# Kernel optimization log

Measured on AMD Instinct MI355X. Metric: run time of the kernel, lower is better.

Reference implementation:

```python
import jax, jax.numpy as jnp
import numpy as np

N = 50000        # nodes
E = 800000       # edges
H = 128          # hidden_channels
NH = 4           # num_heads
HD = H // NH     # head_dim
EPS = 1e-5       # LayerNorm eps (torch default)


def setup_inputs() -> dict:
    key = jax.random.key(0)
    ks = jax.random.split(key, 16)
    s = 0.02
    return {
        "x": jax.random.normal(ks[0], (N, H), dtype=jnp.float32),
        "edge_index": jax.random.randint(ks[1], (2, E), 0, N, dtype=jnp.int64),
        "Wq": jax.random.normal(ks[2], (H, H), dtype=jnp.float32) * s,
        "bq": jnp.zeros((H,), jnp.float32),
        "Wk": jax.random.normal(ks[3], (H, H), dtype=jnp.float32) * s,
        "bk": jnp.zeros((H,), jnp.float32),
        "Wv": jax.random.normal(ks[4], (H, H), dtype=jnp.float32) * s,
        "bv": jnp.zeros((H,), jnp.float32),
        "W1": jax.random.normal(ks[5], (2 * H, H), dtype=jnp.float32) * s,
        "b1": jnp.zeros((H,), jnp.float32),
        "ln_g": jnp.ones((H,), jnp.float32),
        "ln_b": jnp.zeros((H,), jnp.float32),
        "W2": jax.random.normal(ks[6], (H, H), dtype=jnp.float32) * s,
        "b2": jnp.zeros((H,), jnp.float32),
    }


def reference(x, edge_index, Wq, bq, Wk, bk, Wv, bv, W1, b1, ln_g, ln_b, W2, b2):
    n = x.shape[0]
    row, col = edge_index[0], edge_index[1]
    # dense projections, split heads: [N, NH, HD]
    Q = (x @ Wq + bq).reshape(n, NH, HD)
    K = (x @ Wk + bk).reshape(n, NH, HD)
    V = (x @ Wv + bv).reshape(n, NH, HD)
    # edge-wise gather + per-head dot product: [E, NH]
    scores = (Q[row] * K[col]).sum(-1) / jnp.sqrt(jnp.float32(HD))
    # segment softmax over edges grouped by destination node (row)
    m = jax.ops.segment_max(scores, row, num_segments=n)        # [N, NH]
    m = jnp.where(jnp.isfinite(m), m, 0.0)                      # empty segments -> 0
    e = jnp.exp(scores - m[row])                                # [E, NH]
    denom = jax.ops.segment_sum(e, row, num_segments=n)         # [N, NH]
    w = e / denom[row]                                          # [E, NH]
    # weighted scatter-add aggregation: [N, H]
    msg = (w[..., None] * V[col]).reshape(-1, NH * HD)          # [E, H]
    agg = jax.ops.segment_sum(msg, row, num_segments=n)         # [N, H]
    # MLP: Linear -> ReLU -> LayerNorm -> Linear, plus residual
    h = jax.nn.relu(jnp.concatenate([x, agg], axis=-1) @ W1 + b1)
    mu = h.mean(-1, keepdims=True)
    var = ((h - mu) ** 2).mean(-1, keepdims=True)
    h = (h - mu) / jnp.sqrt(var + EPS) * ln_g + ln_b
    return h @ W2 + b2 + x
```

## Files before the change

### kernel.cpp

```cpp
#include <hip/hip_runtime.h>
#include <hip/hip_bf16.h>

#define NN 50000
#define HH 128
#define NHEAD 4
#define HD 32
#define EE 800000
#define LN_EPS 1e-5f
#define ROWS_PAD 50048
#define SCAN_NB 98

typedef __bf16 bf16x8 __attribute__((ext_vector_type(8)));
typedef short  s16x8  __attribute__((ext_vector_type(8)));
typedef float  f32x4  __attribute__((ext_vector_type(4)));

__device__ __forceinline__ f32x4 mfma_bf16(s16x8 a, s16x8 b, f32x4 c) {
    return __builtin_amdgcn_mfma_f32_16x16x32_bf16((bf16x8)a, (bf16x8)b, c, 0, 0, 0);
}

__device__ __forceinline__ unsigned short f2bf(float f) {
    union { float f; unsigned int u; } v; v.f = f;
    unsigned int u = v.u + 0x7FFFu + ((v.u >> 16) & 1u);
    return (unsigned short)(u >> 16);
}

__global__ void detect_idx_kernel(const unsigned int* __restrict__ buf, int* __restrict__ flag) {
    if (blockIdx.x == 0 && threadIdx.x == 0) {
        int is64 = 1;
        for (int i = 0; i < 64; ++i) {
            if (buf[2 * i + 1] != 0u) { is64 = 0; break; }
        }
        *flag = is64;
    }
}

__global__ void convert_hist_kernel(const void* __restrict__ ei, const int* __restrict__ flag,
                                    int* __restrict__ rowi, int* __restrict__ coli,
                                    int* __restrict__ deg) {
    int i = blockIdx.x * blockDim.x + threadIdx.x;
    if (i >= EE) return;
    int r, c;
    if (*flag) {
        const long long* p = (const long long*)ei;
        r = (int)p[i];
        c = (int)p[EE + i];
    } else {
        const int* p = (const int*)ei;
        r = p[i];
        c = p[EE + i];
    }
    rowi[i] = r;
    coli[i] = c;
    atomicAdd(&deg[r], 1);
}

__global__ __launch_bounds__(512) void scan_a_kernel(const int* __restrict__ deg,
                                                     int* __restrict__ bsum) {
    __shared__ int red[8];
    const int t = threadIdx.x;
    const int gid = blockIdx.x * 512 + t;
    int v = (gid < NN) ? deg[gid] : 0;
    #pragma unroll
    for (int o = 1; o < 64; o <<= 1) v += __shfl_xor(v, o);
    if ((t & 63) == 0) red[t >> 6] = v;
    __syncthreads();
    if (t == 0) {
        int s = 0;
        #pragma unroll
        for (int k = 0; k < 8; ++k) s += red[k];
        bsum[blockIdx.x] = s;
    }
}

__global__ void scan_b_kernel(const int* __restrict__ bsum, int* __restrict__ boff) {
    const int lane = threadIdx.x;
    const int i0 = lane * 2, i1 = lane * 2 + 1;
    int a = (i0 < SCAN_NB) ? bsum[i0] : 0;
    int b = (i1 < SCAN_NB) ? bsum[i1] : 0;
    int incl = a + b;
    const int own = incl;
    #pragma unroll
    for (int o = 1; o < 64; o <<= 1) {
        int u = __shfl_up(incl, o);
        if (lane >= o) incl += u;
    }
    int excl = incl - own;
    if (i0 < SCAN_NB) boff[i0] = excl;
    if (i1 < SCAN_NB) boff[i1] = excl + a;
}

__global__ __launch_bounds__(512) void scan_c_kernel(const int* __restrict__ deg,
                                                     const int* __restrict__ boff,
                                                     int* __restrict__ rstart,
                                                     int* __restrict__ cursor) {
    __shared__ int wsum[8];
    const int t = threadIdx.x;
    const int gid = blockIdx.x * 512 + t;
    const int lane = t & 63, w = t >> 6;
    int v = (gid < NN) ? deg[gid] : 0;
    int incl = v;
    #pragma unroll
    for (int o = 1; o < 64; o <<= 1) {
        int u = __shfl_up(incl, o);
        if (lane >= o) incl += u;
    }
    if (lane == 63) wsum[w] = incl;
    __syncthreads();
    int woff = 0;
    for (int k = 0; k < w; ++k) woff += wsum[k];
    int excl = boff[blockIdx.x] + woff + incl - v;
    if (gid < NN) { rstart[gid] = excl; cursor[gid] = excl; }
    if (gid == 0) rstart[NN] = EE;
}

__global__ void scatter_kernel(const int* __restrict__ rowi, const int* __restrict__ coli,
                               int* __restrict__ cursor, int* __restrict__ colS) {
    int i = blockIdx.x * blockDim.x + threadIdx.x;
    if (i >= EE) return;
    int pos = atomicAdd(&cursor[rowi[i]], 1);
    colS[pos] = coli[i];
}

#define PACKX_T 1600000
__global__ void pack_kernel(const float* __restrict__ x,
                            const float* __restrict__ Wq, const float* __restrict__ Wk,
                            const float* __restrict__ Wv, const float* __restrict__ W1,
                            const float* __restrict__ W2,
                            unsigned short* __restrict__ xa, unsigned short* __restrict__ wf) {
    int t = blockIdx.x * blockDim.x + threadIdx.x;
    if (t < PACKX_T) {
        int r = t >> 5;
        int c4 = (t & 31) << 2;
        float4 v = *(const float4*)(x + (size_t)r * HH + c4);
        ushort4 o;
        o.x = f2bf(v.x); o.y = f2bf(v.y); o.z = f2bf(v.z); o.w = f2bf(v.w);
        *(ushort4*)(xa + (size_t)r * 256 + c4) = o;
        return;
    }
    int i = t - PACKX_T;
    if (i >= 98304) return;
    float val;
    if (i < 49152) {
        int j = i & 7, lane = (i >> 3) & 63, kk = (i >> 9) & 3, nt = i >> 11;
        int k = kk * 32 + (lane >> 4) * 8 + j;
        int n = nt * 16 + (lane & 15);
        const float* W = (n < 128) ? Wq : ((n < 256) ? Wk : Wv);
        val = W[k * HH + (n & 127)];
    } else if (i < 81920) {
        int local = i - 49152;
        int j = local & 7, lane = (local >> 3) & 63, kk = (local >> 9) & 7, nt = local >> 12;
        int k = kk * 32 + (lane >> 4) * 8 + j;
        int n = nt * 16 + (lane & 15);
        val = W1[k * HH + n];
    } else {
        int local = i - 81920;
        int j = local & 7, lane = (local >> 3) & 63, kk = (local >> 9) & 3, nt = local >> 11;
        int k = kk * 32 + (lane >> 4) * 8 + j;
        int n = nt * 16 + (lane & 15);
        val = W2[k * HH + n];
    }
    wf[i] = f2bf(val);
}

__global__ __launch_bounds__(256) void gemm_qkv_kernel(
        const unsigned short* __restrict__ xa, const unsigned short* __restrict__ wf,
        const float* __restrict__ bq, const float* __restrict__ bk, const float* __restrict__ bv,
        unsigned short* __restrict__ Qb, unsigned short* __restrict__ Kb,
        unsigned short* __restrict__ Vb) {
    const int wave = threadIdx.x >> 6, lane = threadIdx.x & 63;
    const int row0 = blockIdx.x * 64 + wave * 16;
    const int arow = row0 + (lane & 15);

    s16x8 a[4];
    const unsigned short* ap = xa + (size_t)arow * 256 + (lane >> 4) * 8;
    #pragma unroll
    for (int kk = 0; kk < 4; ++kk) a[kk] = *(const s16x8*)(ap + kk * 32);

    f32x4 acc[24];
    #pragma unroll
    for (int nt = 0; nt < 24; ++nt) acc[nt] = (f32x4){0.f, 0.f, 0.f, 0.f};

    const s16x8* wfv = (const s16x8*)wf;
    #pragma unroll
    for (int nt = 0; nt < 24; ++nt) {
        #pragma unroll
        for (int kk = 0; kk < 4; ++kk) {
            s16x8 b = wfv[(nt * 4 + kk) * 64 + lane];
            acc[nt] = mfma_bf16(a[kk], b, acc[nt]);
        }
    }

    const int colb = lane & 15;
    const int rbase = row0 + (lane >> 4) * 4;
    #pragma unroll
    for (int nt = 0; nt < 24; ++nt) {
        const int mtx = nt >> 3;
        const int nc = (nt & 7) * 16 + colb;
        const float* bias_p = (mtx == 0) ? bq : ((mtx == 1) ? bk : bv);
        unsigned short* O = (mtx == 0) ? Qb : ((mtx == 1) ? Kb : Vb);
        float bias = bias_p[nc];
        #pragma unroll
        for (int r = 0; r < 4; ++r)
            O[(size_t)(rbase + r) * 128 + nc] = f2bf(acc[nt][r] + bias);
    }
}

__global__ __launch_bounds__(256) void attn_kernel(
        const unsigned short* __restrict__ Qb, const unsigned short* __restrict__ Kb,
        const unsigned short* __restrict__ Vb, const int* __restrict__ rstart,
        const int* __restrict__ colS, unsigned short* __restrict__ xa) {
    const int wave = threadIdx.x >> 6;
    const int lane = threadIdx.x & 63;
    const int i = blockIdx.x * 4 + wave;
    if (i >= NN) return;
    const int h = lane & 3;
    const int le = lane >> 2;
    const int g = lane >> 4;
    const int e0 = rstart[i], e1 = rstart[i + 1];
    const int deg = e1 - e0;

    float qf[32];
    {
        const uint4* qp = (const uint4*)(Qb + (size_t)i * 128 + h * 32);
        #pragma unroll
        for (int cch = 0; cch < 4; ++cch) {
            uint4 qv = qp[cch];
            unsigned int w_[4] = {qv.x, qv.y, qv.z, qv.w};
            #pragma unroll
            for (int dd = 0; dd < 4; ++dd) {
                qf[cch * 8 + dd * 2]     = __uint_as_float(w_[dd] << 16);
                qf[cch * 8 + dd * 2 + 1] = __uint_as_float(w_[dd] & 0xffff0000u);
            }
        }
    }

    float m = -INFINITY, l = 0.f;
    float accx = 0.f, accy = 0.f;

    for (int c0 = 0; c0 < deg; c0 += 16) {
        const int cnt = min(16, deg - c0);
        int col = 0;
        float s = -INFINITY;
        if (le < cnt) {
            col = colS[e0 + c0 + le];
            const uint4* kp = (const uint4*)(Kb + (size_t)col * 128 + h * 32);
            float dot = 0.f;
            #pragma unroll
            for (int cch = 0; cch < 4; ++cch) {
                uint4 kv = kp[cch];
                unsigned int w_[4] = {kv.x, kv.y, kv.z, kv.w};
                #pragma unroll
                for (int dd = 0; dd < 4; ++dd) {
                    dot += qf[cch * 8 + dd * 2]     * __uint_as_float(w_[dd] << 16);
                    dot += qf[cch * 8 + dd * 2 + 1] * __uint_as_float(w_[dd] & 0xffff0000u);
                }
            }
            s = dot * 0.17677669529663689f;
        }
        float sm = s;
        sm = fmaxf(sm, __shfl_xor(sm, 4));
        sm = fmaxf(sm, __shfl_xor(sm, 8));
        sm = fmaxf(sm, __shfl_xor(sm, 16));
        sm = fmaxf(sm, __shfl_xor(sm, 32));
        const float mn = fmaxf(m, sm);
        const float p = (le < cnt) ? __expf(s - mn) : 0.f;
        float ps = p;
        ps += __shfl_xor(ps, 4);
        ps += __shfl_xor(ps, 8);
        ps += __shfl_xor(ps, 16);
        ps += __shfl_xor(ps, 32);
        const float fac = __expf(m - mn);
        l = l * fac + ps;
        m = mn;
        const float facbc = __shfl(fac, g);
        accx *= facbc;
        accy *= facbc;
        #pragma unroll
        for (int e = 0; e < 16; ++e) {
            const int   cbc = __shfl(col, 4 * e);
            const float pbc = __shfl(p, 4 * e + g);
            const unsigned int v2 =
                *(const unsigned int*)(Vb + (size_t)cbc * 128 + 2 * lane);
            accx += pbc * __uint_as_float(v2 << 16);
            accy += pbc * __uint_as_float(v2 & 0xffff0000u);
        }
    }

    const float lf = __shfl(l, g);
    const float rinv = (lf > 0.f) ? 1.f / lf : 0.f;
    const unsigned int outw =
        ((unsigned int)f2bf(accy * rinv) << 16) | (unsigned int)f2bf(accx * rinv);
    *(unsigned int*)(xa + (size_t)i * 256 + 128 + 2 * lane) = outw;
}

__global__ __launch_bounds__(256) void gemm_mlp1_kernel(
        const unsigned short* __restrict__ xa, const unsigned short* __restrict__ w1f,
        const float* __restrict__ b1, const float* __restrict__ ln_g,
        const float* __restrict__ ln_b, unsigned short* __restrict__ hb) {
    const int wave = threadIdx.x >> 6, lane = threadIdx.x & 63;
    const int row0 = blockIdx.x * 64 + wave * 16;
    const int arow = row0 + (lane & 15);

    s16x8 a[8];
    const unsigned short* ap = xa + (size_t)arow * 256 + (lane >> 4) * 8;
    #pragma unroll
    for (int kk = 0; kk < 8; ++kk) a[kk] = *(const s16x8*)(ap + kk * 32);

    f32x4 acc[8];
    #pragma unroll
    for (int nt = 0; nt < 8; ++nt) acc[nt] = (f32x4){0.f, 0.f, 0.f, 0.f};

    const s16x8* wfv = (const s16x8*)w1f;
    #pragma unroll
    for (int nt = 0; nt < 8; ++nt) {
        #pragma unroll
        for (int kk = 0; kk < 8; ++kk) {
            s16x8 b = wfv[(nt * 8 + kk) * 64 + lane];
            acc[nt] = mfma_bf16(a[kk], b, acc[nt]);
        }
    }

    const int colb = lane & 15;
    #pragma unroll
    for (int nt = 0; nt < 8; ++nt) {
        float bias = b1[nt * 16 + colb];
        #pragma unroll
        for (int r = 0; r < 4; ++r) {
            float v = acc[nt][r] + bias;
            acc[nt][r] = v > 0.f ? v : 0.f;
        }
    }
    float mu[4], rs[4];
    #pragma unroll
    for (int r = 0; r < 4; ++r) {
        float s = 0.f, q = 0.f;
        #pragma unroll
        for (int nt = 0; nt < 8; ++nt) { float v = acc[nt][r]; s += v; q += v * v; }
        #pragma unroll
        for (int msk = 1; msk < 16; msk <<= 1) {
            s += __shfl_xor(s, msk, 16);
            q += __shfl_xor(q, msk, 16);
        }
        float m_ = s * (1.f / 128.f);
        float var = q * (1.f / 128.f) - m_ * m_;
        mu[r] = m_;
        rs[r] = rsqrtf(var + LN_EPS);
    }
    const int rbase = row0 + (lane >> 4) * 4;
    #pragma unroll
    for (int nt = 0; nt < 8; ++nt) {
        int col = nt * 16 + colb;
        float g = ln_g[col], bb = ln_b[col];
        #pragma unroll
        for (int r = 0; r < 4; ++r) {
            float h = (acc[nt][r] - mu[r]) * rs[r] * g + bb;
            hb[(size_t)(rbase + r) * 128 + col] = f2bf(h);
        }
    }
}

__global__ __launch_bounds__(256) void gemm_mlp2_kernel(
        const unsigned short* __restrict__ hb, const unsigned short* __restrict__ w2f,
        const float* __restrict__ b2, const float* __restrict__ x,
        float* __restrict__ out) {
    const int wave = threadIdx.x >> 6, lane = threadIdx.x & 63;
    const int row0 = blockIdx.x * 64 + wave * 16;
    const int arow = row0 + (lane & 15);

    s16x8 a[4];
    const unsigned short* ap = hb + (size_t)arow * 128 + (lane >> 4) * 8;
    #pragma unroll
    for (int kk = 0; kk < 4; ++kk) a[kk] = *(const s16x8*)(ap + kk * 32);

    f32x4 acc[8];
    #pragma unroll
    for (int nt = 0; nt < 8; ++nt) acc[nt] = (f32x4){0.f, 0.f, 0.f, 0.f};

    const s16x8* wfv = (const s16x8*)w2f;
    #pragma unroll
    for (int nt = 0; nt < 8; ++nt) {
        #pragma unroll
        for (int kk = 0; kk < 4; ++kk) {
            s16x8 b = wfv[(nt * 4 + kk) * 64 + lane];
            acc[nt] = mfma_bf16(a[kk], b, acc[nt]);
        }
    }

    const int colb = lane & 15;
    const int rbase = row0 + (lane >> 4) * 4;
    #pragma unroll
    for (int nt = 0; nt < 8; ++nt) {
        int col = nt * 16 + colb;
        float bias = b2[col];
        #pragma unroll
        for (int r = 0; r < 4; ++r) {
            int row = rbase + r;
            if (row < NN)
                out[(size_t)row * 128 + col] = acc[nt][r] + bias + x[(size_t)row * 128 + col];
        }
    }
}

extern "C" void kernel_launch(void* const* d_in, const int* in_sizes, int n_in,
                              void* d_out, int out_size, void* d_ws, size_t ws_size,
                              hipStream_t stream) {
    const float* x    = (const float*)d_in[0];
    const void*  ei   = d_in[1];
    const float* Wq   = (const float*)d_in[2];
    const float* bq   = (const float*)d_in[3];
    const float* Wk   = (const float*)d_in[4];
    const float* bk   = (const float*)d_in[5];
    const float* Wv   = (const float*)d_in[6];
    const float* bv   = (const float*)d_in[7];
    const float* W1   = (const float*)d_in[8];
    const float* b1   = (const float*)d_in[9];
    const float* ln_g = (const float*)d_in[10];
    const float* ln_b = (const float*)d_in[11];
    const float* W2   = (const float*)d_in[12];
    const float* b2   = (const float*)d_in[13];
    float* out = (float*)d_out;

    char* ws = (char*)d_ws;
    size_t off = 0;
    auto alloc = [&](size_t bytes) {
        size_t o = off;
        off = (off + bytes + 255) & ~(size_t)255;
        return o;
    };
    size_t flag_o = alloc(sizeof(int));
    size_t rowi_o = alloc((size_t)EE * sizeof(int));
    size_t coli_o = alloc((size_t)EE * sizeof(int));
    size_t deg_o  = alloc((size_t)NN * sizeof(int));
    size_t cur_o  = alloc((size_t)NN * sizeof(int));
    size_t rs_o   = alloc((size_t)(NN + 1) * sizeof(int));
    size_t bsum_o = alloc((size_t)SCAN_NB * sizeof(int));
    size_t boff_o = alloc((size_t)SCAN_NB * sizeof(int));
    size_t colS_o = alloc((size_t)EE * sizeof(int));
    size_t xa_o   = alloc((size_t)ROWS_PAD * 256 * sizeof(unsigned short));
    size_t wf_o   = alloc((size_t)98304 * sizeof(unsigned short));
    size_t Qb_o   = alloc((size_t)ROWS_PAD * 128 * sizeof(unsigned short));
    size_t Kb_o   = alloc((size_t)ROWS_PAD * 128 * sizeof(unsigned short));
    size_t Vb_o   = alloc((size_t)ROWS_PAD * 128 * sizeof(unsigned short));
    size_t hb_o   = Qb_o;

    int* flag   = (int*)(ws + flag_o);
    int* rowi   = (int*)(ws + rowi_o);
    int* coli   = (int*)(ws + coli_o);
    int* deg    = (int*)(ws + deg_o);
    int* cursor = (int*)(ws + cur_o);
    int* rstart = (int*)(ws + rs_o);
    int* bsum   = (int*)(ws + bsum_o);
    int* boff   = (int*)(ws + boff_o);
    int* colS   = (int*)(ws + colS_o);
    unsigned short* xa = (unsigned short*)(ws + xa_o);
    unsigned short* wf = (unsigned short*)(ws + wf_o);
    unsigned short* Qb = (unsigned short*)(ws + Qb_o);
    unsigned short* Kb = (unsigned short*)(ws + Kb_o);
    unsigned short* Vb = (unsigned short*)(ws + Vb_o);
    unsigned short* hb = (unsigned short*)(ws + hb_o);

    hipMemsetAsync(ws + deg_o, 0, (size_t)NN * sizeof(int), stream);

    detect_idx_kernel<<<1, 64, 0, stream>>>((const unsigned int*)ei, flag);
    convert_hist_kernel<<<(EE + 255) / 256, 256, 0, stream>>>(ei, flag, rowi, coli, deg);
    scan_a_kernel<<<SCAN_NB, 512, 0, stream>>>(deg, bsum);
    scan_b_kernel<<<1, 64, 0, stream>>>(bsum, boff);
    scan_c_kernel<<<SCAN_NB, 512, 0, stream>>>(deg, boff, rstart, cursor);
    scatter_kernel<<<(EE + 255) / 256, 256, 0, stream>>>(rowi, coli, cursor, colS);

    pack_kernel<<<(PACKX_T + 98304 + 255) / 256, 256, 0, stream>>>(
        x, Wq, Wk, Wv, W1, W2, xa, wf);

    gemm_qkv_kernel<<<ROWS_PAD / 64, 256, 0, stream>>>(xa, wf, bq, bk, bv, Qb, Kb, Vb);

    attn_kernel<<<(NN + 3) / 4, 256, 0, stream>>>(Qb, Kb, Vb, rstart, colS, xa);

    gemm_mlp1_kernel<<<ROWS_PAD / 64, 256, 0, stream>>>(xa, wf + 49152, b1, ln_g, ln_b, hb);

    gemm_mlp2_kernel<<<ROWS_PAD / 64, 256, 0, stream>>>(hb, wf + 81920, b2, x, out);
}
```

Measured before the change: 233.3 us.

## Fuse x bf16 conversion into QKV GEMM, widen edge conversion and V gather

The x-to-bf16 packing now happens inside the QKV GEMM, which writes xa as it reads x, so the separate pass over x is gone. Only the weight packing stays as a standalone kernel. Edge-index conversion handles two edges per thread with vector loads. The attention aggregation splits the wave into two halves that each gather 8-byte V chunks for alternate edges and then combine with a cross-half shuffle. The residual in the final GEMM now reads bf16 x from xa instead of fp32 x, which cuts bandwidth but lowers the residual's precision.

```diff
diff --git a/kernel.cpp b/kernel.cpp
--- a/kernel.cpp
+++ b/kernel.cpp
@@ -23,6 +23,12 @@
     unsigned int u = v.u + 0x7FFFu + ((v.u >> 16) & 1u);
     return (unsigned short)(u >> 16);
 }
+__device__ __forceinline__ float bf2f(unsigned short h) {
+    union { unsigned int u; float f; } v; v.u = ((unsigned int)h) << 16;
+    return v.f;
+}
+__device__ __forceinline__ float bflo(unsigned int w) { return __uint_as_float(w << 16); }
+__device__ __forceinline__ float bfhi(unsigned int w) { return __uint_as_float(w & 0xffff0000u); }
 
 __global__ void detect_idx_kernel(const unsigned int* __restrict__ buf, int* __restrict__ flag) {
     if (blockIdx.x == 0 && threadIdx.x == 0) {
@@ -37,21 +43,26 @@
 __global__ void convert_hist_kernel(const void* __restrict__ ei, const int* __restrict__ flag,
                                     int* __restrict__ rowi, int* __restrict__ coli,
                                     int* __restrict__ deg) {
-    int i = blockIdx.x * blockDim.x + threadIdx.x;
+    int i = (blockIdx.x * blockDim.x + threadIdx.x) * 2;
     if (i >= EE) return;
-    int r, c;
+    int r0, r1, c0, c1;
     if (*flag) {
-        const long long* p = (const long long*)ei;
-        r = (int)p[i];
-        c = (int)p[EE + i];
+        const longlong2* pr = (const longlong2*)((const long long*)ei + i);
+        const longlong2* pc = (const longlong2*)((const long long*)ei + EE + i);
+        longlong2 rv = *pr, cv = *pc;
+        r0 = (int)rv.x; r1 = (int)rv.y;
+        c0 = (int)cv.x; c1 = (int)cv.y;
     } else {
-        const int* p = (const int*)ei;
-        r = p[i];
-        c = p[EE + i];
-    }
-    rowi[i] = r;
-    coli[i] = c;
-    atomicAdd(&deg[r], 1);
+        const int2* pr = (const int2*)((const int*)ei + i);
+        const int2* pc = (const int2*)((const int*)ei + EE + i);
+        int2 rv = *pr, cv = *pc;
+        r0 = rv.x; r1 = rv.y;
+        c0 = cv.x; c1 = cv.y;
+    }
+    *(int2*)(rowi + i) = make_int2(r0, r1);
+    *(int2*)(coli + i) = make_int2(c0, c1);
+    atomicAdd(&deg[r0], 1);
+    atomicAdd(&deg[r1], 1);
 }
 
 __global__ __launch_bounds__(512) void scan_a_kernel(const int* __restrict__ deg,
@@ -121,23 +132,10 @@
     colS[pos] = coli[i];
 }
 
-#define PACKX_T 1600000
-__global__ void pack_kernel(const float* __restrict__ x,
-                            const float* __restrict__ Wq, const float* __restrict__ Wk,
-                            const float* __restrict__ Wv, const float* __restrict__ W1,
-                            const float* __restrict__ W2,
-                            unsigned short* __restrict__ xa, unsigned short* __restrict__ wf) {
-    int t = blockIdx.x * blockDim.x + threadIdx.x;
-    if (t < PACKX_T) {
-        int r = t >> 5;
-        int c4 = (t & 31) << 2;
-        float4 v = *(const float4*)(x + (size_t)r * HH + c4);
-        ushort4 o;
-        o.x = f2bf(v.x); o.y = f2bf(v.y); o.z = f2bf(v.z); o.w = f2bf(v.w);
-        *(ushort4*)(xa + (size_t)r * 256 + c4) = o;
-        return;
-    }
-    int i = t - PACKX_T;
+__global__ void pack_w_kernel(const float* __restrict__ Wq, const float* __restrict__ Wk,
+                              const float* __restrict__ Wv, const float* __restrict__ W1,
+                              const float* __restrict__ W2, unsigned short* __restrict__ wf) {
+    int i = blockIdx.x * blockDim.x + threadIdx.x;
     if (i >= 98304) return;
     float val;
     if (i < 49152) {
@@ -162,19 +160,36 @@
     wf[i] = f2bf(val);
 }
 
-__global__ __launch_bounds__(256) void gemm_qkv_kernel(
-        const unsigned short* __restrict__ xa, const unsigned short* __restrict__ wf,
+__global__ __launch_bounds__(256) void qkvx_kernel(
+        const float* __restrict__ x, const unsigned short* __restrict__ wf,
         const float* __restrict__ bq, const float* __restrict__ bk, const float* __restrict__ bv,
+        unsigned short* __restrict__ xa,
         unsigned short* __restrict__ Qb, unsigned short* __restrict__ Kb,
         unsigned short* __restrict__ Vb) {
     const int wave = threadIdx.x >> 6, lane = threadIdx.x & 63;
     const int row0 = blockIdx.x * 64 + wave * 16;
     const int arow = row0 + (lane & 15);
+    const int kbase = (lane >> 4) * 8;
 
     s16x8 a[4];
-    const unsigned short* ap = xa + (size_t)arow * 256 + (lane >> 4) * 8;
-    #pragma unroll
-    for (int kk = 0; kk < 4; ++kk) a[kk] = *(const s16x8*)(ap + kk * 32);
+    if (arow < NN) {
+        const float* xp = x + (size_t)arow * HH + kbase;
+        #pragma unroll
+        for (int kk = 0; kk < 4; ++kk) {
+            float4 f0 = *(const float4*)(xp + kk * 32);
+            float4 f1 = *(const float4*)(xp + kk * 32 + 4);
+            s16x8 av;
+            av[0] = (short)f2bf(f0.x); av[1] = (short)f2bf(f0.y);
+            av[2] = (short)f2bf(f0.z); av[3] = (short)f2bf(f0.w);
+            av[4] = (short)f2bf(f1.x); av[5] = (short)f2bf(f1.y);
+            av[6] = (short)f2bf(f1.z); av[7] = (short)f2bf(f1.w);
+            a[kk] = av;
+            *(s16x8*)(xa + (size_t)arow * 256 + kbase + kk * 32) = av;
+        }
+    } else {
+        #pragma unroll
+        for (int kk = 0; kk < 4; ++kk) a[kk] = (s16x8)0;
+    }
 
     f32x4 acc[24];
     #pragma unroll
@@ -215,7 +230,9 @@
     if (i >= NN) return;
     const int h = lane & 3;
     const int le = lane >> 2;
-    const int g = lane >> 4;
+    const int half = lane >> 5;
+    const int sl = lane & 31;
+    const int g2 = sl >> 3;
     const int e0 = rstart[i], e1 = rstart[i + 1];
     const int deg = e1 - e0;
 
@@ -228,14 +245,14 @@
             unsigned int w_[4] = {qv.x, qv.y, qv.z, qv.w};
             #pragma unroll
             for (int dd = 0; dd < 4; ++dd) {
-                qf[cch * 8 + dd * 2]     = __uint_as_float(w_[dd] << 16);
-                qf[cch * 8 + dd * 2 + 1] = __uint_as_float(w_[dd] & 0xffff0000u);
+                qf[cch * 8 + dd * 2]     = bflo(w_[dd]);
+                qf[cch * 8 + dd * 2 + 1] = bfhi(w_[dd]);
             }
         }
     }
 
     float m = -INFINITY, l = 0.f;
-    float accx = 0.f, accy = 0.f;
+    float acc0 = 0.f, acc1 = 0.f, acc2 = 0.f, acc3 = 0.f;
 
     for (int c0 = 0; c0 < deg; c0 += 16) {
         const int cnt = min(16, deg - c0);
@@ -251,8 +268,8 @@
                 unsigned int w_[4] = {kv.x, kv.y, kv.z, kv.w};
                 #pragma unroll
                 for (int dd = 0; dd < 4; ++dd) {
-                    dot += qf[cch * 8 + dd * 2]     * __uint_as_float(w_[dd] << 16);
-                    dot += qf[cch * 8 + dd * 2 + 1] * __uint_as_float(w_[dd] & 0xffff0000u);
+                    dot += qf[cch * 8 + dd * 2]     * bflo(w_[dd]);
+                    dot += qf[cch * 8 + dd * 2 + 1] * bfhi(w_[dd]);
                 }
             }
             s = dot * 0.17677669529663689f;
@@ -272,25 +289,33 @@
         const float fac = __expf(m - mn);
         l = l * fac + ps;
         m = mn;
-        const float facbc = __shfl(fac, g);
-        accx *= facbc;
-        accy *= facbc;
-        #pragma unroll
-        for (int e = 0; e < 16; ++e) {
+        const float facbc = __shfl(fac, g2);
+        acc0 *= facbc; acc1 *= facbc; acc2 *= facbc; acc3 *= facbc;
+        #pragma unroll
+        for (int e2 = 0; e2 < 8; ++e2) {
+            const int e = 2 * e2 + half;
             const int   cbc = __shfl(col, 4 * e);
-            const float pbc = __shfl(p, 4 * e + g);
-            const unsigned int v2 =
-                *(const unsigned int*)(Vb + (size_t)cbc * 128 + 2 * lane);
-            accx += pbc * __uint_as_float(v2 << 16);
-            accy += pbc * __uint_as_float(v2 & 0xffff0000u);
-        }
-    }
-
-    const float lf = __shfl(l, g);
+            const float pbc = __shfl(p, 4 * e + g2);
+            const uint2 v2 = *(const uint2*)(Vb + (size_t)cbc * 128 + 4 * sl);
+            acc0 += pbc * bflo(v2.x);
+            acc1 += pbc * bfhi(v2.x);
+            acc2 += pbc * bflo(v2.y);
+            acc3 += pbc * bfhi(v2.y);
+        }
+    }
+
+    acc0 += __shfl_xor(acc0, 32);
+    acc1 += __shfl_xor(acc1, 32);
+    acc2 += __shfl_xor(acc2, 32);
+    acc3 += __shfl_xor(acc3, 32);
+    const float lf = __shfl(l, g2);
     const float rinv = (lf > 0.f) ? 1.f / lf : 0.f;
-    const unsigned int outw =
-        ((unsigned int)f2bf(accy * rinv) << 16) | (unsigned int)f2bf(accx * rinv);
-    *(unsigned int*)(xa + (size_t)i * 256 + 128 + 2 * lane) = outw;
+    if (half == 0) {
+        uint2 o;
+        o.x = ((unsigned int)f2bf(acc1 * rinv) << 16) | (unsigned int)f2bf(acc0 * rinv);
+        o.y = ((unsigned int)f2bf(acc3 * rinv) << 16) | (unsigned int)f2bf(acc2 * rinv);
+        *(uint2*)(xa + (size_t)i * 256 + 128 + 4 * sl) = o;
+    }
 }
 
 __global__ __launch_bounds__(256) void gemm_mlp1_kernel(
@@ -361,7 +386,7 @@
 
 __global__ __launch_bounds__(256) void gemm_mlp2_kernel(
         const unsigned short* __restrict__ hb, const unsigned short* __restrict__ w2f,
-        const float* __restrict__ b2, const float* __restrict__ x,
+        const float* __restrict__ b2, const unsigned short* __restrict__ xa,
         float* __restrict__ out) {
     const int wave = threadIdx.x >> 6, lane = threadIdx.x & 63;
     const int row0 = blockIdx.x * 64 + wave * 16;
@@ -396,7 +421,8 @@
         for (int r = 0; r < 4; ++r) {
             int row = rbase + r;
             if (row < NN)
-                out[(size_t)row * 128 + col] = acc[nt][r] + bias + x[(size_t)row * 128 + col];
+                out[(size_t)row * 128 + col] =
+                    acc[nt][r] + bias + bf2f(xa[(size_t)row * 256 + col]);
         }
     }
 }
@@ -462,20 +488,19 @@
     hipMemsetAsync(ws + deg_o, 0, (size_t)NN * sizeof(int), stream);
 
     detect_idx_kernel<<<1, 64, 0, stream>>>((const unsigned int*)ei, flag);
-    convert_hist_kernel<<<(EE + 255) / 256, 256, 0, stream>>>(ei, flag, rowi, coli, deg);
+    convert_hist_kernel<<<(EE / 2 + 255) / 256, 256, 0, stream>>>(ei, flag, rowi, coli, deg);
     scan_a_kernel<<<SCAN_NB, 512, 0, stream>>>(deg, bsum);
     scan_b_kernel<<<1, 64, 0, stream>>>(bsum, boff);
     scan_c_kernel<<<SCAN_NB, 512, 0, stream>>>(deg, boff, rstart, cursor);
     scatter_kernel<<<(EE + 255) / 256, 256, 0, stream>>>(rowi, coli, cursor, colS);
 
-    pack_kernel<<<(PACKX_T + 98304 + 255) / 256, 256, 0, stream>>>(
-        x, Wq, Wk, Wv, W1, W2, xa, wf);
-
-    gemm_qkv_kernel<<<ROWS_PAD / 64, 256, 0, stream>>>(xa, wf, bq, bk, bv, Qb, Kb, Vb);
+    pack_w_kernel<<<98304 / 256, 256, 0, stream>>>(Wq, Wk, Wv, W1, W2, wf);
+
+    qkvx_kernel<<<ROWS_PAD / 64, 256, 0, stream>>>(x, wf, bq, bk, bv, xa, Qb, Kb, Vb);
 
     attn_kernel<<<(NN + 3) / 4, 256, 0, stream>>>(Qb, Kb, Vb, rstart, colS, xa);
 
     gemm_mlp1_kernel<<<ROWS_PAD / 64, 256, 0, stream>>>(xa, wf + 49152, b1, ln_g, ln_b, hb);
 
-    gemm_mlp2_kernel<<<ROWS_PAD / 64, 256, 0, stream>>>(hb, wf + 81920, b2, x, out);
-}
+    gemm_mlp2_kernel<<<ROWS_PAD / 64, 256, 0, stream>>>(hb, wf + 81920, b2, xa, out);
+}
```

After: 224.1 us. -3.9%, faster.
